# Kernel tuning notes

Measured on AMD Instinct MI355X. Metric: run time of the kernel, lower is better.

## Reference

```python
import jax, jax.numpy as jnp
import numpy as np
from jax import lax

B, T, V, E, H, C = 16, 1024, 256, 512, 1024, 256


def lstm_layer(x, h0, c0, Wih, Whh, bih, bhh):
    """Single unidirectional LSTM layer, batch_first. x: (B,T,I). Returns (ys,(h,c)).
    Torch gate order: i, f, g, o. Input projection hoisted out of the scan (one big GEMM)."""
    xg = jnp.einsum('bti,gi->btg', x, Wih) + (bih + bhh)  # (B,T,4H)

    def step(carry, xt):
        h, c = carry
        gates = xt + h @ Whh.T
        i, f, g, o = jnp.split(gates, 4, axis=-1)
        c = jax.nn.sigmoid(f) * c + jax.nn.sigmoid(i) * jnp.tanh(g)
        h = jax.nn.sigmoid(o) * jnp.tanh(c)
        return (h, c), h

    (h, c), ys = lax.scan(step, (h0, c0), jnp.swapaxes(xg, 0, 1))
    return jnp.swapaxes(ys, 0, 1), h, c


def run_stack(emb_tokens, h0s, c0s, layers):
    """layers: list of (Wih, Whh, bih, bhh). h0s/c0s: (L,B,H)."""
    x = emb_tokens
    hs, cs = [], []
    for l, (Wih, Whh, bih, bhh) in enumerate(layers):
        x, h, c = lstm_layer(x, h0s[l], c0s[l], Wih, Whh, bih, bhh)
        hs.append(h)
        cs.append(c)
    return x, jnp.stack(hs), jnp.stack(cs)


def setup_inputs() -> dict:
    key = jax.random.key(0)
    ks = iter(jax.random.split(key, 32))
    s = 1.0 / np.sqrt(H)

    def u(shape):
        return jax.random.uniform(next(ks), shape, jnp.float32, -s, s)

    inp = {"x": jax.random.randint(next(ks), (B, T), 0, V)}
    inp["enc_emb"] = jax.random.normal(next(ks), (V, E), jnp.float32)
    inp["dec_emb"] = jax.random.normal(next(ks), (V, E), jnp.float32)
    for pre in ("enc", "dec"):
        for l in range(2):
            I = E if l == 0 else H
            inp[f"{pre}_Wih{l}"] = u((4 * H, I))
            inp[f"{pre}_Whh{l}"] = u((4 * H, H))
            inp[f"{pre}_bih{l}"] = u((4 * H,))
            inp[f"{pre}_bhh{l}"] = u((4 * H,))
    inp["out_W"] = u((C, H))
    inp["out_b"] = u((C,))
    return inp


def reference(x, enc_emb, dec_emb,
              enc_Wih0, enc_Whh0, enc_bih0, enc_bhh0,
              enc_Wih1, enc_Whh1, enc_bih1, enc_bhh1,
              dec_Wih0, dec_Whh0, dec_bih0, dec_bhh0,
              dec_Wih1, dec_Whh1, dec_bih1, dec_bhh1,
              out_W, out_b):
    enc_layers = [(enc_Wih0, enc_Whh0, enc_bih0, enc_bhh0),
                  (enc_Wih1, enc_Whh1, enc_bih1, enc_bhh1)]
    dec_layers = [(dec_Wih0, dec_Whh0, dec_bih0, dec_bhh0),
                  (dec_Wih1, dec_Whh1, dec_bih1, dec_bhh1)]
    L = len(enc_layers)
    z = jnp.zeros((L, x.shape[0], H), jnp.float32)
    # Encoder (dropout is identity at inference)
    _, h, c = run_stack(enc_emb[x], z, z, enc_layers)
    # Decoder with teacher forcing on the same tokens
    dec_out, _, _ = run_stack(dec_emb[x], h, c, dec_layers)
    logits = dec_out @ out_W.T + out_b  # (B,T,C)
    return jnp.swapaxes(logits, 1, 2)   # (B,C,T)
```

## Files before the change

kernel.cpp:

```cpp
#include <hip/hip_runtime.h>
#include <stdint.h>

#define B_  16
#define T_  1024
#define H_  1024
#define E_  512
#define V_  256
#define C_  256

typedef __bf16 bf16x8 __attribute__((ext_vector_type(8)));
typedef float  f32x4  __attribute__((ext_vector_type(4)));
typedef unsigned short u16;
typedef unsigned int   u32;
typedef unsigned long long u64;

__device__ __forceinline__ float bf2f(u16 u) {
  union { unsigned int i; float f; } v; v.i = ((unsigned int)u) << 16; return v.f;
}
__device__ __forceinline__ u16 f2bf(float f) {
  union { float f; unsigned int i; } v; v.f = f;
  unsigned int u = v.i;
  return (u16)((u + 0x7fffu + ((u >> 16) & 1u)) >> 16);
}
__device__ __forceinline__ bf16x8 ld_bf8(const u16* p) {
  uint4 v = *(const uint4*)p;
  return __builtin_bit_cast(bf16x8, v);
}
__device__ __forceinline__ float sigm(float x) { return 1.f / (1.f + __expf(-x)); }

__device__ __forceinline__ bf16x8 ldw8(const void* W, size_t off, bool f32in) {
  if (f32in) {
    const float* p = (const float*)W + off;
    float4 a = *(const float4*)p;
    float4 b = *(const float4*)(p + 4);
    union { u16 s[8]; bf16x8 v; } r;
    r.s[0]=f2bf(a.x); r.s[1]=f2bf(a.y); r.s[2]=f2bf(a.z); r.s[3]=f2bf(a.w);
    r.s[4]=f2bf(b.x); r.s[5]=f2bf(b.y); r.s[6]=f2bf(b.z); r.s[7]=f2bf(b.w);
    return r.v;
  }
  return ld_bf8((const u16*)W + off);
}
__device__ __forceinline__ float ldb1(const void* p, int i, bool f32in) {
  return f32in ? ((const float*)p)[i] : bf2f(((const u16*)p)[i]);
}

__global__ void probe_k(const u16* __restrict__ s, int* __restrict__ flag) {
  if (threadIdx.x == 0) {
    int cnt = 0;
    for (int i = 0; i < 256; ++i) {
      int e = (s[i] >> 7) & 0xFF;
      if (e >= 124) ++cnt;
    }
    flag[0] = (cnt >= 16) ? 1 : 0;
  }
}

__global__ void cvt_k(const void* __restrict__ src, u16* __restrict__ dst, int n,
                      const int* __restrict__ flagp) {
  int i = blockIdx.x * blockDim.x + threadIdx.x;
  if (i >= n) return;
  if (*flagp) dst[i] = f2bf(((const float*)src)[i]);
  else        dst[i] = ((const u16*)src)[i];
}

struct PersistArgs {
  const int* tok;
  const u16 *eemb, *demb;
  const void *Wih[4], *Whh[4], *bih[4], *bhh[4];
  u16 *zslot;
  u16 *he0[2], *he1[2], *hd0[2], *hd1[2];
  u16 *seq;
  u32 *flags;
  const int *dflag;
};

struct PhaseP {
  const void *Wx, *Wh, *bi, *bh;
  const u16* emb;
  const int* tok;
  u16 *r0[2], *r1[2];
  const u16 *h0init, *h1init;
  u16* seq;
  u32* flags;
  bool f32in, init_c;
  int c0, bid, tid;
  u32 gp0;
};

__device__ __forceinline__ void gbar(u32* flags, int bid, int tid, u32 gp) {
  __syncthreads();
  if (tid == 0)
    __hip_atomic_store(&flags[bid], gp, __ATOMIC_RELAXED, __HIP_MEMORY_SCOPE_AGENT);
  if (tid < 256) {
    while (__hip_atomic_load(&flags[tid], __ATOMIC_RELAXED, __HIP_MEMORY_SCOPE_AGENT) < gp)
      __builtin_amdgcn_s_sleep(2);
  }
  if (tid == 0)
    (void)__hip_atomic_load(&flags[0], __ATOMIC_ACQUIRE, __HIP_MEMORY_SCOPE_AGENT);
  __syncthreads();
}

template<int LAYER>
__device__ u32 run_phase(const PhaseP& q, f32x4* red4, float* gbuf, float* cbuf,
                         float* bbuf, u16* hstage) {
  constexpr int KX = LAYER ? 1024 : 512;
  constexpr int NX = KX / 256;
  const int tid = q.tid, w = tid >> 6, l = tid & 63;
  const int rr = l & 15, ksub = (l >> 4) * 8;

  bf16x8 BX[2][NX], BH[2][4];
  #pragma unroll
  for (int t = 0; t < 2; ++t) {
    const size_t row = (size_t)((t * 2 + (rr >> 3)) * 1024 + q.c0 + (rr & 7));
    #pragma unroll
    for (int it = 0; it < NX; ++it)
      BX[t][it] = ldw8(q.Wx, row * KX + w * (KX / 8) + it * 32 + ksub, q.f32in);
    #pragma unroll
    for (int it = 0; it < 4; ++it)
      BH[t][it] = ldw8(q.Wh, row * 1024 + w * 128 + it * 32 + ksub, q.f32in);
  }
  if (tid < 32) {
    const int row = (tid >> 3) * 1024 + q.c0 + (tid & 7);
    bbuf[tid] = ldb1(q.bi, row, q.f32in) + ldb1(q.bh, row, q.f32in);
  }
  if (q.init_c && tid < 128) cbuf[tid] = 0.f;
  __syncthreads();

  int tok_cur = (LAYER == 0) ? q.tok[rr * T_ + 0] : 0;
  u32 gp = q.gp0;

  for (int s = 0; s <= T_; ++s) {
    const bool active = (LAYER == 0) ? (s < T_) : (s >= 1);
    if (active) {
      const u16* xrow;
      const u16* hrow;
      if (LAYER == 0) {
        xrow = q.emb + (size_t)tok_cur * 512;
        hrow = (s == 0) ? (q.h0init + rr * H_) : (q.r0[(s - 1) & 1] + rr * H_);
      } else {
        xrow = q.r0[(s - 1) & 1] + rr * H_;
        hrow = (s == 1) ? (q.h1init + rr * H_) : (q.r1[s & 1] + rr * H_);
      }
      f32x4 a0 = {0.f,0.f,0.f,0.f}, a1 = {0.f,0.f,0.f,0.f};
      #pragma unroll
      for (int it = 0; it < NX; ++it) {
        bf16x8 a = ld_bf8(xrow + w * (KX / 8) + it * 32 + ksub);
        a0 = __builtin_amdgcn_mfma_f32_16x16x32_bf16(a, BX[0][it], a0, 0, 0, 0);
        a1 = __builtin_amdgcn_mfma_f32_16x16x32_bf16(a, BX[1][it], a1, 0, 0, 0);
      }
      #pragma unroll
      for (int it = 0; it < 4; ++it) {
        bf16x8 a = ld_bf8(hrow + w * 128 + it * 32 + ksub);
        a0 = __builtin_amdgcn_mfma_f32_16x16x32_bf16(a, BH[0][it], a0, 0, 0, 0);
        a1 = __builtin_amdgcn_mfma_f32_16x16x32_bf16(a, BH[1][it], a1, 0, 0, 0);
      }
      red4[(w * 2 + 0) * 64 + l] = a0;
      red4[(w * 2 + 1) * 64 + l] = a1;
    }
    if (LAYER == 0) {
      const int tn = (s + 1 < T_) ? (s + 1) : (T_ - 1);
      tok_cur = q.tok[rr * T_ + tn];
    }
    __syncthreads();
    if (active && tid < 128) {
      const int tt = tid >> 6, ll = tid & 63;
      f32x4 ssum = {0.f,0.f,0.f,0.f};
      #pragma unroll
      for (int w8 = 0; w8 < 8; ++w8) ssum += red4[(w8 * 2 + tt) * 64 + ll];
      const int n = ll & 15, gate = tt * 2 + (n >> 3), j = n & 7, mg = (ll >> 4) * 4;
      const float bsum = bbuf[gate * 8 + j];
      #pragma unroll
      for (int r = 0; r < 4; ++r) gbuf[(gate * 8 + j) * 17 + mg + r] = ssum[r] + bsum;
    }
    __syncthreads();
    if (active && tid < 128) {
      const int j = tid >> 4, m = tid & 15;
      const float iv = sigm(gbuf[(0  + j) * 17 + m]);
      const float fv = sigm(gbuf[(8  + j) * 17 + m]);
      const float gv = tanhf(gbuf[(16 + j) * 17 + m]);
      const float ov = sigm(gbuf[(24 + j) * 17 + m]);
      const float cn = fv * cbuf[j * 16 + m] + iv * gv;
      cbuf[j * 16 + m] = cn;
      hstage[m * 8 + j] = f2bf(ov * tanhf(cn));
    }
    __syncthreads();
    if (active && tid < 32) {
      const int m = tid >> 1, half = tid & 1;
      const u64 v = ((const u64*)hstage)[m * 2 + half];
      u16* outs = (LAYER == 0) ? q.r0[s & 1] : q.r1[(s - 1) & 1];
      __hip_atomic_store((u64*)(outs + m * H_ + q.c0 + half * 4), v,
                         __ATOMIC_RELAXED, __HIP_MEMORY_SCOPE_AGENT);
      if (q.seq) {
        const int t = s - 1;
        __hip_atomic_store((u64*)(q.seq + ((size_t)m * T_ + t) * H_ + q.c0 + half * 4),
                           v, __ATOMIC_RELAXED, __HIP_MEMORY_SCOPE_AGENT);
      }
    }
    gbar(q.flags, q.bid, tid, gp);
    ++gp;
  }
  return gp;
}

__global__ __launch_bounds__(512, 2) void persist_k(PersistArgs P) {
  __shared__ f32x4 red4[16 * 64];
  __shared__ float gbuf[544];
  __shared__ float cbuf[128];
  __shared__ float bbuf[32];
  __shared__ u16   hstage[128];
  const int bid = blockIdx.x, tid = threadIdx.x;
  const int layer = bid >> 7;
  const int c0 = (bid & 127) * 8;
  const bool f32in = (*P.dflag != 0);

  u32 gp = 1;
  for (int ph = 0; ph < 2; ++ph) {
    PhaseP q;
    const int wi = ph * 2 + layer;
    q.Wx = P.Wih[wi]; q.Wh = P.Whh[wi]; q.bi = P.bih[wi]; q.bh = P.bhh[wi];
    q.emb = ph ? P.demb : P.eemb;
    q.tok = P.tok;
    q.r0[0] = ph ? P.hd0[0] : P.he0[0]; q.r0[1] = ph ? P.hd0[1] : P.he0[1];
    q.r1[0] = ph ? P.hd1[0] : P.he1[0]; q.r1[1] = ph ? P.hd1[1] : P.he1[1];
    q.h0init = ph ? P.he0[1] : P.zslot;
    q.h1init = ph ? P.he1[1] : P.zslot;
    q.seq = (ph == 1 && layer == 1) ? P.seq : nullptr;
    q.flags = P.flags;
    q.f32in = f32in; q.init_c = (ph == 0);
    q.c0 = c0; q.bid = bid; q.tid = tid; q.gp0 = gp;
    gp = layer ? run_phase<1>(q, red4, gbuf, cbuf, bbuf, hstage)
               : run_phase<0>(q, red4, gbuf, cbuf, bbuf, hstage);
  }
}

__global__ __launch_bounds__(256) void logits_k(const u16* __restrict__ A,
                                                const u16* __restrict__ W,
                                                const u16* __restrict__ bias,
                                                void* __restrict__ out,
                                                const int* __restrict__ dflag) {
  const int wid  = blockIdx.x * 4 + (threadIdx.x >> 6);
  const int mt   = wid >> 4;
  const int nt   = wid & 15;
  const int lane = threadIdx.x & 63;
  const int l15  = lane & 15;
  const int quad = lane >> 4;
  const int ko   = quad * 8;
  const u16* arow = A + (size_t)(mt * 16 + l15) * H_;
  const u16* brow = W + (size_t)(nt * 16 + l15) * H_;
  f32x4 acc = {0.f,0.f,0.f,0.f};
  #pragma unroll 4
  for (int kk = 0; kk < H_; kk += 32) {
    acc = __builtin_amdgcn_mfma_f32_16x16x32_bf16(ld_bf8(arow + kk + ko),
                                                  ld_bf8(brow + kk + ko), acc, 0, 0, 0);
  }
  const int c  = nt * 16 + l15;
  const float bv = bf2f(bias[c]);
  const int f32out = *dflag;
  #pragma unroll
  for (int r = 0; r < 4; ++r) {
    const int m = mt * 16 + quad * 4 + r;
    const int b = m >> 10, t = m & 1023;
    const size_t idx = ((size_t)b * C_ + c) * T_ + t;
    const float v = acc[r] + bv;
    if (f32out) ((float*)out)[idx] = v;
    else        ((u16*)out)[idx]   = f2bf(v);
  }
}

extern "C" void kernel_launch(void* const* d_in, const int* in_sizes, int n_in,
                              void* d_out, int out_size, void* d_ws, size_t ws_size,
                              hipStream_t stream) {
  (void)in_sizes; (void)n_in; (void)out_size; (void)ws_size;

  const int* x = (const int*)d_in[0];

  char* ws = (char*)d_ws;
  u32* flags  = (u32*)ws;
  u16* zslot  = (u16*)(ws + 16384);
  int* dflag  = (int*)(ws + 49152);
  char* base  = ws + 49408;
  size_t ob = 0;
  u16* p_eemb = (u16*)(base + ob); ob += (size_t)V_ * E_ * 2;
  u16* p_demb = (u16*)(base + ob); ob += (size_t)V_ * E_ * 2;
  u16* p_outW = (u16*)(base + ob); ob += (size_t)C_ * H_ * 2;
  u16* p_outb = (u16*)(base + ob); ob += 512;
  u16* rings  = (u16*)(base + ob); ob += 8 * (size_t)B_ * H_ * 2;
  u16* seq    = (u16*)(base + ob); ob += (size_t)B_ * T_ * H_ * 2;
  const size_t SLOT = (size_t)B_ * H_;

  hipMemsetAsync(ws, 0, 49408, stream);

  probe_k<<<1, 64, 0, stream>>>((const u16*)d_in[5], dflag);

  cvt_k<<<(V_ * E_ + 255) / 256, 256, 0, stream>>>(d_in[1], p_eemb, V_ * E_, dflag);
  cvt_k<<<(V_ * E_ + 255) / 256, 256, 0, stream>>>(d_in[2], p_demb, V_ * E_, dflag);
  cvt_k<<<(C_ * H_ + 255) / 256, 256, 0, stream>>>(d_in[19], p_outW, C_ * H_, dflag);
  cvt_k<<<1, 256, 0, stream>>>(d_in[20], p_outb, C_, dflag);

  PersistArgs P;
  P.tok = x; P.eemb = p_eemb; P.demb = p_demb;
  for (int l = 0; l < 4; ++l) {
    P.Wih[l] = d_in[3 + 4 * l + 0];
    P.Whh[l] = d_in[3 + 4 * l + 1];
    P.bih[l] = d_in[3 + 4 * l + 2];
    P.bhh[l] = d_in[3 + 4 * l + 3];
  }
  P.zslot = zslot;
  P.he0[0] = rings + 0 * SLOT; P.he0[1] = rings + 1 * SLOT;
  P.he1[0] = rings + 2 * SLOT; P.he1[1] = rings + 3 * SLOT;
  P.hd0[0] = rings + 4 * SLOT; P.hd0[1] = rings + 5 * SLOT;
  P.hd1[0] = rings + 6 * SLOT; P.hd1[1] = rings + 7 * SLOT;
  P.seq = seq; P.flags = flags; P.dflag = dflag;

  persist_k<<<256, 512, 0, stream>>>(P);

  logits_k<<<4096, 256, 0, stream>>>(seq, p_outW, p_outb, d_out, dflag);
}
```

Measured before the change: 16.42 ms.

## Use master-block broadcast grid barrier and write hidden state directly

Replaces the all-to-all grid barrier, where each block polled all 256 flags, with a centralized one: block 0 gathers the flags and then publishes a single broadcast word that the other blocks poll. This cuts global polling traffic per timestep but adds an extra hop of latency through block 0. It also drops the shared-memory staging of h and the extra __syncthreads by having each thread store its bf16 value directly, at the cost of narrower 16-bit atomic stores instead of 64-bit ones.

```diff
diff --git a/kernel.cpp b/kernel.cpp
--- a/kernel.cpp
+++ b/kernel.cpp
@@ -71,6 +71,7 @@
   u16 *he0[2], *he1[2], *hd0[2], *hd1[2];
   u16 *seq;
   u32 *flags;
+  u32 *bcast;
   const int *dflag;
 };
 
@@ -81,28 +82,39 @@
   u16 *r0[2], *r1[2];
   const u16 *h0init, *h1init;
   u16* seq;
-  u32* flags;
+  u32 *flags, *bcast;
   bool f32in, init_c;
   int c0, bid, tid;
   u32 gp0;
 };
 
-__device__ __forceinline__ void gbar(u32* flags, int bid, int tid, u32 gp) {
+__device__ __forceinline__ void gbar(u32* flags, u32* bcast, int bid, int tid, u32 gp) {
   __syncthreads();
-  if (tid == 0)
-    __hip_atomic_store(&flags[bid], gp, __ATOMIC_RELAXED, __HIP_MEMORY_SCOPE_AGENT);
-  if (tid < 256) {
-    while (__hip_atomic_load(&flags[tid], __ATOMIC_RELAXED, __HIP_MEMORY_SCOPE_AGENT) < gp)
-      __builtin_amdgcn_s_sleep(2);
-  }
-  if (tid == 0)
-    (void)__hip_atomic_load(&flags[0], __ATOMIC_ACQUIRE, __HIP_MEMORY_SCOPE_AGENT);
-  __syncthreads();
+  if (bid == 0) {
+    if (tid >= 1 && tid < 256) {
+      while (__hip_atomic_load(&flags[tid], __ATOMIC_RELAXED, __HIP_MEMORY_SCOPE_AGENT) < gp)
+        __builtin_amdgcn_s_sleep(1);
+    }
+    __syncthreads();
+    if (tid == 0) {
+      (void)__hip_atomic_load(&flags[0], __ATOMIC_ACQUIRE, __HIP_MEMORY_SCOPE_AGENT);
+      __hip_atomic_store(bcast, gp, __ATOMIC_RELAXED, __HIP_MEMORY_SCOPE_AGENT);
+    }
+    __syncthreads();
+  } else {
+    if (tid == 0) {
+      __hip_atomic_store(&flags[bid], gp, __ATOMIC_RELAXED, __HIP_MEMORY_SCOPE_AGENT);
+      while (__hip_atomic_load(bcast, __ATOMIC_RELAXED, __HIP_MEMORY_SCOPE_AGENT) < gp)
+        __builtin_amdgcn_s_sleep(1);
+      (void)__hip_atomic_load(&flags[0], __ATOMIC_ACQUIRE, __HIP_MEMORY_SCOPE_AGENT);
+    }
+    __syncthreads();
+  }
 }
 
 template<int LAYER>
 __device__ u32 run_phase(const PhaseP& q, f32x4* red4, float* gbuf, float* cbuf,
-                         float* bbuf, u16* hstage) {
+                         float* bbuf) {
   constexpr int KX = LAYER ? 1024 : 512;
   constexpr int NX = KX / 256;
   const int tid = q.tid, w = tid >> 6, l = tid & 63;
@@ -181,22 +193,17 @@
       const float ov = sigm(gbuf[(24 + j) * 17 + m]);
       const float cn = fv * cbuf[j * 16 + m] + iv * gv;
       cbuf[j * 16 + m] = cn;
-      hstage[m * 8 + j] = f2bf(ov * tanhf(cn));
-    }
-    __syncthreads();
-    if (active && tid < 32) {
-      const int m = tid >> 1, half = tid & 1;
-      const u64 v = ((const u64*)hstage)[m * 2 + half];
+      const u16 hv = f2bf(ov * tanhf(cn));
       u16* outs = (LAYER == 0) ? q.r0[s & 1] : q.r1[(s - 1) & 1];
-      __hip_atomic_store((u64*)(outs + m * H_ + q.c0 + half * 4), v,
+      __hip_atomic_store(outs + m * H_ + q.c0 + j, hv,
                          __ATOMIC_RELAXED, __HIP_MEMORY_SCOPE_AGENT);
       if (q.seq) {
         const int t = s - 1;
-        __hip_atomic_store((u64*)(q.seq + ((size_t)m * T_ + t) * H_ + q.c0 + half * 4),
-                           v, __ATOMIC_RELAXED, __HIP_MEMORY_SCOPE_AGENT);
+        __hip_atomic_store(q.seq + ((size_t)m * T_ + t) * H_ + q.c0 + j, hv,
+                           __ATOMIC_RELAXED, __HIP_MEMORY_SCOPE_AGENT);
       }
     }
-    gbar(q.flags, q.bid, tid, gp);
+    gbar(q.flags, q.bcast, q.bid, tid, gp);
     ++gp;
   }
   return gp;
@@ -207,7 +214,6 @@
   __shared__ float gbuf[544];
   __shared__ float cbuf[128];
   __shared__ float bbuf[32];
-  __shared__ u16   hstage[128];
   const int bid = blockIdx.x, tid = threadIdx.x;
   const int layer = bid >> 7;
   const int c0 = (bid & 127) * 8;
@@ -225,11 +231,11 @@
     q.h0init = ph ? P.he0[1] : P.zslot;
     q.h1init = ph ? P.he1[1] : P.zslot;
     q.seq = (ph == 1 && layer == 1) ? P.seq : nullptr;
-    q.flags = P.flags;
+    q.flags = P.flags; q.bcast = P.bcast;
     q.f32in = f32in; q.init_c = (ph == 0);
     q.c0 = c0; q.bid = bid; q.tid = tid; q.gp0 = gp;
-    gp = layer ? run_phase<1>(q, red4, gbuf, cbuf, bbuf, hstage)
-               : run_phase<0>(q, red4, gbuf, cbuf, bbuf, hstage);
+    gp = layer ? run_phase<1>(q, red4, gbuf, cbuf, bbuf)
+               : run_phase<0>(q, red4, gbuf, cbuf, bbuf);
   }
 }
 
@@ -276,6 +282,7 @@
 
   char* ws = (char*)d_ws;
   u32* flags  = (u32*)ws;
+  u32* bcast  = (u32*)(ws + 8192);
   u16* zslot  = (u16*)(ws + 16384);
   int* dflag  = (int*)(ws + 49152);
   char* base  = ws + 49408;
@@ -310,7 +317,7 @@
   P.he1[0] = rings + 2 * SLOT; P.he1[1] = rings + 3 * SLOT;
   P.hd0[0] = rings + 4 * SLOT; P.hd0[1] = rings + 5 * SLOT;
   P.hd1[0] = rings + 6 * SLOT; P.hd1[1] = rings + 7 * SLOT;
-  P.seq = seq; P.flags = flags; P.dflag = dflag;
+  P.seq = seq; P.flags = flags; P.bcast = bcast; P.dflag = dflag;
 
   persist_k<<<256, 512, 0, stream>>>(P);
 
```

After: 15.60 ms. 1.05x faster.
